# Kernel optimization log

Hardware: AMD Instinct MI355X
Metric: run time of the kernel (lower is better)

Reference implementation:

```python
import jax, jax.numpy as jnp
import numpy as np

B, S, D = 2, 2048, 1024
H, DH = 16, 64
WINDOW = 256


def setup_inputs() -> dict:
    key = jax.random.key(0)
    ks = jax.random.split(key, 11)
    s = 1.0 / np.sqrt(D)
    return {
        "query": jax.random.normal(ks[0], (B, S, D), jnp.float32),
        "key": jax.random.normal(ks[1], (B, S, D), jnp.float32),
        "value": jax.random.normal(ks[2], (B, S, D), jnp.float32),
        "Wq": jax.random.normal(ks[3], (D, D), jnp.float32) * s,
        "bq": jax.random.normal(ks[4], (D,), jnp.float32) * s,
        "Wk": jax.random.normal(ks[5], (D, D), jnp.float32) * s,
        "bk": jax.random.normal(ks[6], (D,), jnp.float32) * s,
        "Wv": jax.random.normal(ks[7], (D, D), jnp.float32) * s,
        "bv": jax.random.normal(ks[8], (D,), jnp.float32) * s,
        "Wo": jax.random.normal(ks[9], (D, D), jnp.float32) * s,
        "bo": jax.random.normal(ks[10], (D,), jnp.float32) * s,
    }


def reference(query, key, value, Wq, bq, Wk, bk, Wv, bv, Wo, bo):
    scale = DH ** -0.5
    # projections (torch Linear: x @ W.T + b)
    q = query @ Wq.T + bq  # [B,S,D]
    k = key @ Wk.T + bk
    v = value @ Wv.T + bv
    # split heads -> [B,H,S,DH]
    q = q.reshape(B, S, H, DH).transpose(0, 2, 1, 3)
    k = k.reshape(B, S, H, DH).transpose(0, 2, 1, 3)
    v = v.reshape(B, S, H, DH).transpose(0, 2, 1, 3)
    # dense scores with sliding-window causal mask
    attn = jnp.einsum('bhqd,bhkd->bhqk', q, k) * scale  # [B,H,S,S]
    q_idx = jnp.arange(S)[:, None]
    k_idx = jnp.arange(S)[None, :]
    keep = (k_idx <= q_idx) & (k_idx >= q_idx - WINDOW + 1)  # causal & window
    attn = jnp.where(keep[None, None], attn, -jnp.inf)
    attn = jax.nn.softmax(attn, axis=-1)
    # dropout_p=0.0 (eval) -> identity
    out = jnp.einsum('bhqk,bhkd->bhqd', attn, v)  # [B,H,S,DH]
    out = out.transpose(0, 2, 1, 3).reshape(B, S, D)
    return out @ Wo.T + bo
```

## Files before the change

### kernel.cpp

```cpp
#include <hip/hip_runtime.h>
#include <cstdint>
#include <cstddef>

#define B_   2
#define S_   2048
#define D_   1024
#define H_   16
#define DH_  64
#define NROW (B_ * S_)

typedef __bf16  bf16x8 __attribute__((ext_vector_type(8)));
typedef __bf16  bf16x4 __attribute__((ext_vector_type(4)));
typedef float   f32x4  __attribute__((ext_vector_type(4)));

#define MFMA16(a, b, c) __builtin_amdgcn_mfma_f32_16x16x32_bf16((a), (b), (c), 0, 0, 0)

__device__ __forceinline__ void gload_lds16(const void* g, void* l) {
  __builtin_amdgcn_global_load_lds(
      (__attribute__((address_space(1))) void*)(g),
      (__attribute__((address_space(3))) void*)(l), 16, 0, 0);
}

struct Ptr3 { const float* p[3]; };
struct Ptr4 { const float* p[4]; };

__global__ void cast3(Ptr3 src, __bf16* dst, int n4each) {
  const int i = blockIdx.x * blockDim.x + threadIdx.x;
  const float4 v = ((const float4*)src.p[blockIdx.y])[i];
  bf16x4 o; o[0] = (__bf16)v.x; o[1] = (__bf16)v.y; o[2] = (__bf16)v.z; o[3] = (__bf16)v.w;
  ((bf16x4*)dst)[(size_t)blockIdx.y * n4each + i] = o;
}
__global__ void cast4(Ptr4 src, __bf16* dst, int n4each) {
  const int i = blockIdx.x * blockDim.x + threadIdx.x;
  const float4 v = ((const float4*)src.p[blockIdx.y])[i];
  bf16x4 o; o[0] = (__bf16)v.x; o[1] = (__bf16)v.y; o[2] = (__bf16)v.z; o[3] = (__bf16)v.w;
  ((bf16x4*)dst)[(size_t)blockIdx.y * n4each + i] = o;
}

struct QKVArgs {
  const __bf16* A[3]; const __bf16* W[3]; const float* bias[3]; __bf16* C[3];
};

__global__ __launch_bounds__(256, 2) void gemm_qkv(QKVArgs args) {
  __shared__ __bf16 As[128 * 32];
  __shared__ __bf16 Bs[128 * 32];
  const int z = blockIdx.z;
  const __bf16* A = args.A[z];
  const __bf16* W = args.W[z];
  const float* bias = args.bias[z];
  __bf16* C = args.C[z];
  const int tid  = threadIdx.x;
  const int lane = tid & 63, wave = tid >> 6;
  const int lo   = lane & 15, quad = lane >> 4;
  const int wr   = wave & 1,  wc   = wave >> 1;
  const int bn   = blockIdx.x, bm = blockIdx.y;
  const __bf16* Ag = A + (size_t)bn * 128 * D_;
  const __bf16* Wg = W + (size_t)bm * 128 * D_;
  const int c0 = tid, c1 = tid + 256;
  const int r0 = c0 >> 2, s0 = (c0 & 3) * 8;
  const int r1 = c1 >> 2, s1 = (c1 & 3) * 8;

  f32x4 acc[4][4] = {};
  for (int k0 = 0; k0 < D_; k0 += 32) {
    __syncthreads();
    gload_lds16(Ag + (size_t)r0 * D_ + k0 + s0, &As[c0 * 8]);
    gload_lds16(Ag + (size_t)r1 * D_ + k0 + s1, &As[c1 * 8]);
    gload_lds16(Wg + (size_t)r0 * D_ + k0 + s0, &Bs[c0 * 8]);
    gload_lds16(Wg + (size_t)r1 * D_ + k0 + s1, &Bs[c1 * 8]);
    __syncthreads();
    bf16x8 af[4], bfr[4];
#pragma unroll
    for (int i = 0; i < 4; i++)
      af[i] = *(const bf16x8*)&As[(wr * 64 + i * 16 + lo) * 32 + quad * 8];
#pragma unroll
    for (int j = 0; j < 4; j++)
      bfr[j] = *(const bf16x8*)&Bs[(wc * 64 + j * 16 + lo) * 32 + quad * 8];
#pragma unroll
    for (int i = 0; i < 4; i++)
#pragma unroll
      for (int j = 0; j < 4; j++)
        acc[i][j] = MFMA16(af[i], bfr[j], acc[i][j]);
  }
  if (z == 2) {
#pragma unroll
    for (int i = 0; i < 4; i++) {
      const int row0 = bn * 128 + wr * 64 + i * 16 + quad * 4;
      const int bb = row0 >> 11, s = row0 & (S_ - 1);
#pragma unroll
      for (int j = 0; j < 4; j++) {
        const int col = bm * 128 + wc * 64 + j * 16 + lo;
        const int hh = col >> 6, dd = col & 63;
        const float bv = bias[col];
        bf16x4 o;
#pragma unroll
        for (int r = 0; r < 4; r++) o[r] = (__bf16)(acc[i][j][r] + bv);
        *(bf16x4*)&C[((size_t)(bb * H_ + hh) * DH_ + dd) * S_ + s] = o;
      }
    }
  } else {
#pragma unroll
    for (int i = 0; i < 4; i++) {
      const int row = bn * 128 + wr * 64 + i * 16 + quad * 4;
#pragma unroll
      for (int j = 0; j < 4; j++) {
        const int col = bm * 128 + wc * 64 + j * 16 + lo;
        const float bv = bias[col];
#pragma unroll
        for (int r = 0; r < 4; r++)
          C[(size_t)(row + r) * D_ + col] = (__bf16)(acc[i][j][r] + bv);
      }
    }
  }
}

__global__ __launch_bounds__(256, 2) void attn_win2(
    const __bf16* __restrict__ Qp, const __bf16* __restrict__ Kp,
    const __bf16* __restrict__ Vt, __bf16* __restrict__ ctx) {
  __shared__ __bf16 Qs[64 * 64];
  __shared__ __bf16 Ks[5][64 * 64];
  __shared__ __bf16 Vs[2][64 * 64];
  __shared__ __bf16 Pb[4][16 * 72];
  const int qt = blockIdx.x, h = blockIdx.y, b = blockIdx.z;
  const int q0 = qt * 64;
  const int tid = threadIdx.x, wave = tid >> 6, lane = tid & 63;
  const int lo = lane & 15, quad = lane >> 4;
  const int tmin = (q0 >= 256) ? 0 : ((256 - q0) >> 6);
  const __bf16* Qg = Qp + ((size_t)b * S_ + q0) * D_ + h * DH_;
  const __bf16* Kg = Kp + (size_t)b * S_ * D_ + h * DH_;
  const __bf16* Vg = Vt + (size_t)(b * H_ + h) * DH_ * S_;

  const int c0 = tid, c1 = tid + 256;
  const int rA = c0 >> 3, gA = ((c0 & 7) ^ (rA & 7)) * 8;
  const int rB = c1 >> 3, gB = ((c1 & 7) ^ (rB & 7)) * 8;

  auto stageV = [&](int t) {
    const int k0 = q0 - 256 + t * 64;
    gload_lds16(Vg + (size_t)rA * S_ + k0 + gA, &Vs[t & 1][c0 * 8]);
    gload_lds16(Vg + (size_t)rB * S_ + k0 + gB, &Vs[t & 1][c1 * 8]);
  };

  gload_lds16(Qg + (size_t)rA * D_ + gA, &Qs[c0 * 8]);
  gload_lds16(Qg + (size_t)rB * D_ + gB, &Qs[c1 * 8]);
#pragma unroll
  for (int t = 0; t < 5; t++) {
    if (t < tmin) continue;
    const int k0 = q0 - 256 + t * 64;
    gload_lds16(Kg + (size_t)(k0 + rA) * D_ + gA, &Ks[t][c0 * 8]);
    gload_lds16(Kg + (size_t)(k0 + rB) * D_ + gB, &Ks[t][c1 * 8]);
  }
  stageV(tmin);
  if (tmin + 1 <= 4) stageV(tmin + 1);
  __syncthreads();

  const int g0 = (quad ^ (lo & 7)) * 8;
  const int g1 = ((quad + 4) ^ (lo & 7)) * 8;

  const int qrow = wave * 16 + lo;
  const bf16x8 qf0 = *(const bf16x8*)&Qs[qrow * 64 + g0];
  const bf16x8 qf1 = *(const bf16x8*)&Qs[qrow * 64 + g1];
  f32x4 sc[5][4];
#pragma unroll
  for (int t = 0; t < 5; t++) {
    if (t < tmin) continue;
#pragma unroll
    for (int kt = 0; kt < 4; kt++) {
      const int kr = kt * 16 + lo;
      const bf16x8 kf0 = *(const bf16x8*)&Ks[t][kr * 64 + g0];
      const bf16x8 kf1 = *(const bf16x8*)&Ks[t][kr * 64 + g1];
      f32x4 c = {0.f, 0.f, 0.f, 0.f};
      c = MFMA16(qf0, kf0, c);
      c = MFMA16(qf1, kf1, c);
      sc[t][kt] = c;
    }
  }

  const float scale = 0.125f;
  const int dbase = lo - wave * 16 - quad * 4 - 256;
  float mrow[4] = {-3e38f, -3e38f, -3e38f, -3e38f};
#pragma unroll
  for (int t = 0; t < 5; t++) {
    if (t < tmin) continue;
#pragma unroll
    for (int kt = 0; kt < 4; kt++)
#pragma unroll
      for (int r = 0; r < 4; r++) {
        const int delta = dbase + t * 64 + kt * 16 - r;
        const bool keep = (delta <= 0) && (delta > -256);
        const float v = keep ? sc[t][kt][r] * scale : -3e38f;
        sc[t][kt][r] = v;
        mrow[r] = fmaxf(mrow[r], v);
      }
  }
#pragma unroll
  for (int r = 0; r < 4; r++)
#pragma unroll
    for (int off = 1; off < 16; off <<= 1)
      mrow[r] = fmaxf(mrow[r], __shfl_xor(mrow[r], off));

  float lrow[4] = {0.f, 0.f, 0.f, 0.f};
#pragma unroll
  for (int t = 0; t < 5; t++) {
    if (t < tmin) continue;
#pragma unroll
    for (int kt = 0; kt < 4; kt++)
#pragma unroll
      for (int r = 0; r < 4; r++) {
        const float p = __expf(sc[t][kt][r] - mrow[r]);
        sc[t][kt][r] = p;
        lrow[r] += p;
      }
  }
#pragma unroll
  for (int r = 0; r < 4; r++)
#pragma unroll
    for (int off = 1; off < 16; off <<= 1)
      lrow[r] += __shfl_xor(lrow[r], off);

  f32x4 oacc[4] = {};
#pragma unroll
  for (int t = 0; t < 5; t++) {
    if (t < tmin) continue;
#pragma unroll
    for (int kt = 0; kt < 4; kt++)
#pragma unroll
      for (int r = 0; r < 4; r++)
        Pb[wave][(quad * 4 + r) * 72 + kt * 16 + lo] = (__bf16)sc[t][kt][r];
    const bf16x8 pf0 = *(const bf16x8*)&Pb[wave][lo * 72 + quad * 8];
    const bf16x8 pf1 = *(const bf16x8*)&Pb[wave][lo * 72 + 32 + quad * 8];
#pragma unroll
    for (int ds = 0; ds < 4; ds++) {
      const bf16x8 vf0 = *(const bf16x8*)&Vs[t & 1][(ds * 16 + lo) * 64 + g0];
      const bf16x8 vf1 = *(const bf16x8*)&Vs[t & 1][(ds * 16 + lo) * 64 + g1];
      oacc[ds] = MFMA16(pf0, vf0, oacc[ds]);
      oacc[ds] = MFMA16(pf1, vf1, oacc[ds]);
    }
    if (t < 4) {
      __syncthreads();
      if (t + 2 <= 4) stageV(t + 2);
    }
  }

#pragma unroll
  for (int ds = 0; ds < 4; ds++)
#pragma unroll
    for (int r = 0; r < 4; r++) {
      const int qg = q0 + wave * 16 + quad * 4 + r;
      ctx[((size_t)b * S_ + qg) * D_ + h * DH_ + ds * 16 + lo] =
          (__bf16)(oacc[ds][r] / lrow[r]);
    }
}

__global__ __launch_bounds__(256, 2) void gemm_o(
    const __bf16* __restrict__ A, const __bf16* __restrict__ W,
    const float* __restrict__ bias, float* __restrict__ C) {
  __shared__ __bf16 As[64 * 32];
  __shared__ __bf16 Bs[128 * 32];
  const int tid = threadIdx.x, lane = tid & 63, wave = tid >> 6;
  const int lo = lane & 15, quad = lane >> 4;
  const int wr = wave & 1, wc = wave >> 1;
  const int bn = blockIdx.x, bm = blockIdx.y;
  const __bf16* Ag = A + (size_t)bn * 64 * D_;
  const __bf16* Wg = W + (size_t)bm * 128 * D_;
  const int ra = tid >> 2, sa = (tid & 3) * 8;
  const int cb0 = tid, cb1 = tid + 256;
  const int rb0 = cb0 >> 2, sb0 = (cb0 & 3) * 8;
  const int rb1 = cb1 >> 2, sb1 = (cb1 & 3) * 8;
  f32x4 acc[2][4] = {};
  for (int k0 = 0; k0 < D_; k0 += 32) {
    __syncthreads();
    gload_lds16(Ag + (size_t)ra * D_ + k0 + sa, &As[tid * 8]);
    gload_lds16(Wg + (size_t)rb0 * D_ + k0 + sb0, &Bs[cb0 * 8]);
    gload_lds16(Wg + (size_t)rb1 * D_ + k0 + sb1, &Bs[cb1 * 8]);
    __syncthreads();
    bf16x8 af[2], bfr[4];
#pragma unroll
    for (int i = 0; i < 2; i++)
      af[i] = *(const bf16x8*)&As[(wr * 32 + i * 16 + lo) * 32 + quad * 8];
#pragma unroll
    for (int j = 0; j < 4; j++)
      bfr[j] = *(const bf16x8*)&Bs[(wc * 64 + j * 16 + lo) * 32 + quad * 8];
#pragma unroll
    for (int i = 0; i < 2; i++)
#pragma unroll
      for (int j = 0; j < 4; j++)
        acc[i][j] = MFMA16(af[i], bfr[j], acc[i][j]);
  }
#pragma unroll
  for (int i = 0; i < 2; i++) {
    const int row = bn * 64 + wr * 32 + i * 16 + quad * 4;
#pragma unroll
    for (int j = 0; j < 4; j++) {
      const int col = bm * 128 + wc * 64 + j * 16 + lo;
      const float bv = bias[col];
#pragma unroll
      for (int r = 0; r < 4; r++)
        C[(size_t)(row + r) * D_ + col] = acc[i][j][r] + bv;
    }
  }
}

extern "C" void kernel_launch(void* const* d_in, const int* in_sizes, int n_in,
                              void* d_out, int out_size, void* d_ws, size_t ws_size,
                              hipStream_t stream) {
  (void)in_sizes; (void)n_in; (void)out_size; (void)ws_size;
  const float* q_in = (const float*)d_in[0];
  const float* k_in = (const float*)d_in[1];
  const float* v_in = (const float*)d_in[2];
  const float* Wq   = (const float*)d_in[3];
  const float* bq   = (const float*)d_in[4];
  const float* Wk   = (const float*)d_in[5];
  const float* bk   = (const float*)d_in[6];
  const float* Wv   = (const float*)d_in[7];
  const float* bv   = (const float*)d_in[8];
  const float* Wo   = (const float*)d_in[9];
  const float* bo   = (const float*)d_in[10];

  const size_t XN = (size_t)NROW * D_;
  const size_t WN = (size_t)D_ * D_;
  char* ws = (char*)d_ws;
  __bf16* xq  = (__bf16*)ws; ws += XN * 2;
  __bf16* xk  = (__bf16*)ws; ws += XN * 2;
  __bf16* xv  = (__bf16*)ws; ws += XN * 2;
  __bf16* wqb = (__bf16*)ws; ws += WN * 2;
  __bf16* wkb = (__bf16*)ws; ws += WN * 2;
  __bf16* wvb = (__bf16*)ws; ws += WN * 2;
  __bf16* wob = (__bf16*)ws; ws += WN * 2;
  __bf16* Qp  = (__bf16*)ws; ws += XN * 2;
  __bf16* Kp  = (__bf16*)ws; ws += XN * 2;
  __bf16* Vtp = (__bf16*)ws; ws += XN * 2;
  __bf16* ctx = (__bf16*)ws; ws += XN * 2;

  Ptr3 xs{{q_in, k_in, v_in}};
  Ptr4 wsrc{{Wq, Wk, Wv, Wo}};
  cast3<<<dim3((int)(XN / 4 / 256), 3), 256, 0, stream>>>(xs, xq, (int)(XN / 4));
  cast4<<<dim3((int)(WN / 4 / 256), 4), 256, 0, stream>>>(wsrc, wqb, (int)(WN / 4));

  QKVArgs qa;
  qa.A[0] = xq;  qa.A[1] = xk;  qa.A[2] = xv;
  qa.W[0] = wqb; qa.W[1] = wkb; qa.W[2] = wvb;
  qa.bias[0] = bq; qa.bias[1] = bk; qa.bias[2] = bv;
  qa.C[0] = Qp; qa.C[1] = Kp; qa.C[2] = Vtp;
  gemm_qkv<<<dim3(NROW / 128, D_ / 128, 3), 256, 0, stream>>>(qa);

  attn_win2<<<dim3(S_ / 64, H_, B_), 256, 0, stream>>>(Qp, Kp, Vtp, ctx);

  gemm_o<<<dim3(NROW / 64, D_ / 128), 256, 0, stream>>>(ctx, wob, bo, (float*)d_out);
}
```

Baseline: 198.4 us.

## Alias attention LDS buffers, merge cast launches, raise QKV GEMM occupancy

The attention kernel now uses one flat shared buffer. V tiles are staged into the K region after the score pass, and the P scratch also reuses K space, which shrinks LDS per block. The next P tile is written before the barrier so its store overlaps the sync. The two fp32-to-bf16 cast kernels are merged into a single launch, and gemm_qkv's launch bound is raised to 3 blocks per CU. Delaying V loads until after QK^T removes the overlap of V traffic with score compute, and the tighter launch bound may cause register spills.

```diff
diff --git a/kernel.cpp b/kernel.cpp
--- a/kernel.cpp
+++ b/kernel.cpp
@@ -21,27 +21,24 @@
       (__attribute__((address_space(3))) void*)(l), 16, 0, 0);
 }
 
-struct Ptr3 { const float* p[3]; };
-struct Ptr4 { const float* p[4]; };
-
-__global__ void cast3(Ptr3 src, __bf16* dst, int n4each) {
-  const int i = blockIdx.x * blockDim.x + threadIdx.x;
-  const float4 v = ((const float4*)src.p[blockIdx.y])[i];
-  bf16x4 o; o[0] = (__bf16)v.x; o[1] = (__bf16)v.y; o[2] = (__bf16)v.z; o[3] = (__bf16)v.w;
-  ((bf16x4*)dst)[(size_t)blockIdx.y * n4each + i] = o;
-}
-__global__ void cast4(Ptr4 src, __bf16* dst, int n4each) {
-  const int i = blockIdx.x * blockDim.x + threadIdx.x;
-  const float4 v = ((const float4*)src.p[blockIdx.y])[i];
-  bf16x4 o; o[0] = (__bf16)v.x; o[1] = (__bf16)v.y; o[2] = (__bf16)v.z; o[3] = (__bf16)v.w;
-  ((bf16x4*)dst)[(size_t)blockIdx.y * n4each + i] = o;
+struct CastArgs { const float* src[7]; __bf16* dst[7]; };
+
+__global__ void cast_all(CastArgs a) {
+  int b = blockIdx.x, which, idx;
+  if (b < 12288) { which = b >> 12; idx = b & 4095; }
+  else { b -= 12288; which = 3 + (b >> 10); idx = b & 1023; }
+  const int i = idx * 256 + threadIdx.x;
+  const float4 v = ((const float4*)a.src[which])[i];
+  bf16x4 o;
+  o[0] = (__bf16)v.x; o[1] = (__bf16)v.y; o[2] = (__bf16)v.z; o[3] = (__bf16)v.w;
+  ((bf16x4*)a.dst[which])[i] = o;
 }
 
 struct QKVArgs {
   const __bf16* A[3]; const __bf16* W[3]; const float* bias[3]; __bf16* C[3];
 };
 
-__global__ __launch_bounds__(256, 2) void gemm_qkv(QKVArgs args) {
+__global__ __launch_bounds__(256, 3) void gemm_qkv(QKVArgs args) {
   __shared__ __bf16 As[128 * 32];
   __shared__ __bf16 Bs[128 * 32];
   const int z = blockIdx.z;
@@ -113,13 +110,10 @@
   }
 }
 
-__global__ __launch_bounds__(256, 2) void attn_win2(
+__global__ __launch_bounds__(256, 2) void attn_win3(
     const __bf16* __restrict__ Qp, const __bf16* __restrict__ Kp,
     const __bf16* __restrict__ Vt, __bf16* __restrict__ ctx) {
-  __shared__ __bf16 Qs[64 * 64];
-  __shared__ __bf16 Ks[5][64 * 64];
-  __shared__ __bf16 Vs[2][64 * 64];
-  __shared__ __bf16 Pb[4][16 * 72];
+  __shared__ __bf16 smem[24576];
   const int qt = blockIdx.x, h = blockIdx.y, b = blockIdx.z;
   const int q0 = qt * 64;
   const int tid = threadIdx.x, wave = tid >> 6, lane = tid & 63;
@@ -135,29 +129,28 @@
 
   auto stageV = [&](int t) {
     const int k0 = q0 - 256 + t * 64;
-    gload_lds16(Vg + (size_t)rA * S_ + k0 + gA, &Vs[t & 1][c0 * 8]);
-    gload_lds16(Vg + (size_t)rB * S_ + k0 + gB, &Vs[t & 1][c1 * 8]);
+    const int vb = 4096 + (t & 1) * 4096;
+    gload_lds16(Vg + (size_t)rA * S_ + k0 + gA, &smem[vb + c0 * 8]);
+    gload_lds16(Vg + (size_t)rB * S_ + k0 + gB, &smem[vb + c1 * 8]);
   };
 
-  gload_lds16(Qg + (size_t)rA * D_ + gA, &Qs[c0 * 8]);
-  gload_lds16(Qg + (size_t)rB * D_ + gB, &Qs[c1 * 8]);
+  gload_lds16(Qg + (size_t)rA * D_ + gA, &smem[c0 * 8]);
+  gload_lds16(Qg + (size_t)rB * D_ + gB, &smem[c1 * 8]);
 #pragma unroll
   for (int t = 0; t < 5; t++) {
     if (t < tmin) continue;
     const int k0 = q0 - 256 + t * 64;
-    gload_lds16(Kg + (size_t)(k0 + rA) * D_ + gA, &Ks[t][c0 * 8]);
-    gload_lds16(Kg + (size_t)(k0 + rB) * D_ + gB, &Ks[t][c1 * 8]);
-  }
-  stageV(tmin);
-  if (tmin + 1 <= 4) stageV(tmin + 1);
+    gload_lds16(Kg + (size_t)(k0 + rA) * D_ + gA, &smem[4096 + t * 4096 + c0 * 8]);
+    gload_lds16(Kg + (size_t)(k0 + rB) * D_ + gB, &smem[4096 + t * 4096 + c1 * 8]);
+  }
   __syncthreads();
 
   const int g0 = (quad ^ (lo & 7)) * 8;
   const int g1 = ((quad + 4) ^ (lo & 7)) * 8;
 
   const int qrow = wave * 16 + lo;
-  const bf16x8 qf0 = *(const bf16x8*)&Qs[qrow * 64 + g0];
-  const bf16x8 qf1 = *(const bf16x8*)&Qs[qrow * 64 + g1];
+  const bf16x8 qf0 = *(const bf16x8*)&smem[qrow * 64 + g0];
+  const bf16x8 qf1 = *(const bf16x8*)&smem[qrow * 64 + g1];
   f32x4 sc[5][4];
 #pragma unroll
   for (int t = 0; t < 5; t++) {
@@ -165,14 +158,18 @@
 #pragma unroll
     for (int kt = 0; kt < 4; kt++) {
       const int kr = kt * 16 + lo;
-      const bf16x8 kf0 = *(const bf16x8*)&Ks[t][kr * 64 + g0];
-      const bf16x8 kf1 = *(const bf16x8*)&Ks[t][kr * 64 + g1];
+      const bf16x8 kf0 = *(const bf16x8*)&smem[4096 + t * 4096 + kr * 64 + g0];
+      const bf16x8 kf1 = *(const bf16x8*)&smem[4096 + t * 4096 + kr * 64 + g1];
       f32x4 c = {0.f, 0.f, 0.f, 0.f};
       c = MFMA16(qf0, kf0, c);
       c = MFMA16(qf1, kf1, c);
       sc[t][kt] = c;
     }
   }
+
+  __syncthreads();
+  stageV(tmin);
+  if (tmin + 1 <= 4) stageV(tmin + 1);
 
   const float scale = 0.125f;
   const int dbase = lo - wave * 16 - quad * 4 - 256;
@@ -216,25 +213,33 @@
     for (int off = 1; off < 16; off <<= 1)
       lrow[r] += __shfl_xor(lrow[r], off);
 
+  const int pw = 12288 + wave * 1152;
+  auto writeP = [&](int t) {
+#pragma unroll
+    for (int kt = 0; kt < 4; kt++)
+#pragma unroll
+      for (int r = 0; r < 4; r++)
+        smem[pw + (quad * 4 + r) * 72 + kt * 16 + lo] = (__bf16)sc[t][kt][r];
+  };
+
   f32x4 oacc[4] = {};
-#pragma unroll
-  for (int t = 0; t < 5; t++) {
-    if (t < tmin) continue;
-#pragma unroll
-    for (int kt = 0; kt < 4; kt++)
-#pragma unroll
-      for (int r = 0; r < 4; r++)
-        Pb[wave][(quad * 4 + r) * 72 + kt * 16 + lo] = (__bf16)sc[t][kt][r];
-    const bf16x8 pf0 = *(const bf16x8*)&Pb[wave][lo * 72 + quad * 8];
-    const bf16x8 pf1 = *(const bf16x8*)&Pb[wave][lo * 72 + 32 + quad * 8];
+  writeP(tmin);
+  __syncthreads();
+#pragma unroll
+  for (int t = 0; t < 5; t++) {
+    if (t < tmin) continue;
+    const bf16x8 pf0 = *(const bf16x8*)&smem[pw + lo * 72 + quad * 8];
+    const bf16x8 pf1 = *(const bf16x8*)&smem[pw + lo * 72 + 32 + quad * 8];
+    const int vb = 4096 + (t & 1) * 4096;
 #pragma unroll
     for (int ds = 0; ds < 4; ds++) {
-      const bf16x8 vf0 = *(const bf16x8*)&Vs[t & 1][(ds * 16 + lo) * 64 + g0];
-      const bf16x8 vf1 = *(const bf16x8*)&Vs[t & 1][(ds * 16 + lo) * 64 + g1];
+      const bf16x8 vf0 = *(const bf16x8*)&smem[vb + (ds * 16 + lo) * 64 + g0];
+      const bf16x8 vf1 = *(const bf16x8*)&smem[vb + (ds * 16 + lo) * 64 + g1];
       oacc[ds] = MFMA16(pf0, vf0, oacc[ds]);
       oacc[ds] = MFMA16(pf1, vf1, oacc[ds]);
     }
     if (t < 4) {
+      writeP(t + 1);
       __syncthreads();
       if (t + 2 <= 4) stageV(t + 2);
     }
@@ -330,10 +335,12 @@
   __bf16* Vtp = (__bf16*)ws; ws += XN * 2;
   __bf16* ctx = (__bf16*)ws; ws += XN * 2;
 
-  Ptr3 xs{{q_in, k_in, v_in}};
-  Ptr4 wsrc{{Wq, Wk, Wv, Wo}};
-  cast3<<<dim3((int)(XN / 4 / 256), 3), 256, 0, stream>>>(xs, xq, (int)(XN / 4));
-  cast4<<<dim3((int)(WN / 4 / 256), 4), 256, 0, stream>>>(wsrc, wqb, (int)(WN / 4));
+  CastArgs ca;
+  ca.src[0] = q_in; ca.src[1] = k_in; ca.src[2] = v_in;
+  ca.src[3] = Wq; ca.src[4] = Wk; ca.src[5] = Wv; ca.src[6] = Wo;
+  ca.dst[0] = xq; ca.dst[1] = xk; ca.dst[2] = xv;
+  ca.dst[3] = wqb; ca.dst[4] = wkb; ca.dst[5] = wvb; ca.dst[6] = wob;
+  cast_all<<<16384, 256, 0, stream>>>(ca);
 
   QKVArgs qa;
   qa.A[0] = xq;  qa.A[1] = xk;  qa.A[2] = xv;
@@ -342,7 +349,7 @@
   qa.C[0] = Qp; qa.C[1] = Kp; qa.C[2] = Vtp;
   gemm_qkv<<<dim3(NROW / 128, D_ / 128, 3), 256, 0, stream>>>(qa);
 
-  attn_win2<<<dim3(S_ / 64, H_, B_), 256, 0, stream>>>(Qp, Kp, Vtp, ctx);
+  attn_win3<<<dim3(S_ / 64, H_, B_), 256, 0, stream>>>(Qp, Kp, Vtp, ctx);
 
   gemm_o<<<dim3(NROW / 64, D_ / 128), 256, 0, stream>>>(ctx, wob, bo, (float*)d_out);
 }
```

After: 229.3 us. 1.16x slower.
